# Optimization experiments

Measured on AMD Instinct MI355X. Metric: run time of the kernel, lower is better.

## Reference

```python
import jax, jax.numpy as jnp
import numpy as np

PATCH_NUMS = (10, 20, 30, 40)   # action_dim=10 * (1,2,3,4)
L = sum(PATCH_NUMS)             # 100
FIRST_L = PATCH_NUMS[0]         # 10
C = 768; NH = 12; HD = C // NH; DEPTH = 8; V = 4096; CVAE = 32; OBS = 23; TO = 1
EPS = 1e-6
STD = 0.02

LVL = np.concatenate([np.full(pn, i, dtype=np.int64) for i, pn in enumerate(PATCH_NUMS)])  # [L]
ATTN_BIAS = np.where(LVL[:, None] >= LVL[None, :], 0.0, -np.inf).astype(np.float32)       # [L, L] block-causal


def _ln(x):
    # LayerNorm without affine (eps=1e-6), as in norm_layer(..., elementwise_affine=False)
    m = x.mean(-1, keepdims=True)
    v = ((x - m) ** 2).mean(-1, keepdims=True)
    return (x - m) / jnp.sqrt(v + EPS)


def setup_inputs() -> dict:
    key = jax.random.key(0)
    ks = iter(jax.random.split(key, 40))
    B = 128
    p = {}
    p["nobs"] = jax.random.normal(next(ks), (B, TO, OBS), jnp.float32)
    p["x_BLCv_wo_first_l"] = jax.random.normal(next(ks), (B, L - FIRST_L, CVAE), jnp.float32)
    p["obs_w"] = jax.random.normal(next(ks), (OBS * TO, C), jnp.float32) * STD
    p["obs_b"] = jnp.zeros((C,), jnp.float32)
    p["word_w"] = jax.random.normal(next(ks), (CVAE, C), jnp.float32) * STD
    p["word_b"] = jnp.zeros((C,), jnp.float32)
    p["pos_start"] = jax.random.normal(next(ks), (1, FIRST_L, C), jnp.float32) * STD
    p["pos_1LC"] = jax.random.normal(next(ks), (1, L, C), jnp.float32) * STD
    p["lvl_emb"] = jax.random.normal(next(ks), (len(PATCH_NUMS), C), jnp.float32) * STD
    p["ada_w"] = jax.random.normal(next(ks), (DEPTH, C, 6 * C), jnp.float32) * STD
    p["ada_b"] = jnp.zeros((DEPTH, 6 * C), jnp.float32)
    p["qkv_w"] = jax.random.normal(next(ks), (DEPTH, C, 3 * C), jnp.float32) * STD
    p["qkv_b"] = jnp.zeros((DEPTH, 3 * C), jnp.float32)
    p["proj_w"] = jax.random.normal(next(ks), (DEPTH, C, C), jnp.float32) * STD
    p["proj_b"] = jnp.zeros((DEPTH, C), jnp.float32)
    p["fc1_w"] = jax.random.normal(next(ks), (DEPTH, C, 4 * C), jnp.float32) * STD
    p["fc1_b"] = jnp.zeros((DEPTH, 4 * C), jnp.float32)
    p["fc2_w"] = jax.random.normal(next(ks), (DEPTH, 4 * C, C), jnp.float32) * STD
    p["fc2_b"] = jnp.zeros((DEPTH, C), jnp.float32)
    p["hnm_w"] = jax.random.normal(next(ks), (C, 2 * C), jnp.float32) * STD
    p["hnm_b"] = jnp.zeros((2 * C,), jnp.float32)
    p["head_w"] = jax.random.normal(next(ks), (C, V), jnp.float32) * STD
    p["head_b"] = jnp.zeros((V,), jnp.float32)
    return p


def reference(nobs, x_BLCv_wo_first_l, obs_w, obs_b, word_w, word_b, pos_start, pos_1LC,
              lvl_emb, ada_w, ada_b, qkv_w, qkv_b, proj_w, proj_b, fc1_w, fc1_b,
              fc2_w, fc2_b, hnm_w, hnm_b, head_w, head_b):
    B = x_BLCv_wo_first_l.shape[0]
    feat = nobs[:, :TO].reshape(B, -1)                     # [B, obs_dim*To]
    cond = feat @ obs_w + obs_b                            # [B, C] (= sos = cond_BD)
    sos = cond[:, None, :] + pos_start                     # [B, first_l, C]
    x = jnp.concatenate([sos, x_BLCv_wo_first_l @ word_w + word_b], axis=1)  # [B, L, C]
    x = x + lvl_emb[jnp.asarray(LVL)][None] + pos_1LC      # lvl + positional embed
    bias = jnp.asarray(ATTN_BIAS)                          # [L, L]
    cond_s = jax.nn.silu(cond)                             # shared SiLU input to each block's ada_lin
    scale = HD ** -0.5
    for i in range(DEPTH):
        ada = (cond_s @ ada_w[i] + ada_b[i]).reshape(B, 1, 6, C)
        g1, g2, s1, s2, sh1, sh2 = (ada[:, :, j] for j in range(6))
        h = _ln(x) * (s1 + 1.0) + sh1
        qkv = (h @ qkv_w[i] + qkv_b[i]).reshape(B, L, 3, NH, HD)
        q, k, v = qkv[:, :, 0], qkv[:, :, 1], qkv[:, :, 2]
        att = jnp.einsum('bqhd,bkhd->bhqk', q, k) * scale
        att = jax.nn.softmax(att + bias, axis=-1)
        o = jnp.einsum('bhqk,bkhd->bqhd', att, v).reshape(B, L, C)
        x = x + (o @ proj_w[i] + proj_b[i]) * g1
        h = _ln(x) * (s2 + 1.0) + sh2
        h = jax.nn.gelu(h @ fc1_w[i] + fc1_b[i]) @ fc2_w[i] + fc2_b[i]
        x = x + h * g2
    # AdaLNBeforeHead + head
    hd = (cond_s @ hnm_w + hnm_b).reshape(B, 1, 2, C)
    x = _ln(x) * (hd[:, :, 0] + 1.0) + hd[:, :, 1]
    return x @ head_w + head_b                             # [B, L, V]
```

## Files before the change

### kernel.cpp

```cpp
#include <hip/hip_runtime.h>
#include <hip/hip_bf16.h>

typedef unsigned short u16;
typedef unsigned int u32;
typedef __attribute__((ext_vector_type(8))) short bf16x8;
typedef __attribute__((ext_vector_type(4))) float f32x4;

#define GLDS(gptr, lptr) __builtin_amdgcn_global_load_lds( \
    (const __attribute__((address_space(1))) u32*)(gptr), \
    (__attribute__((address_space(3))) u32*)(lptr), 16, 0, 0)

__device__ __forceinline__ float bf2f(u16 x) {
  union { float f; u32 u; } c; c.u = ((u32)x) << 16; return c.f;
}
__device__ __forceinline__ u16 f2bf(float f) {
  union { float f; u32 u; } c; c.f = f;
  u32 u = c.u;
  return (u16)((u + 0x7FFFu + ((u >> 16) & 1u)) >> 16);
}
__device__ __forceinline__ uint2 pack_bf4(f32x4 v) {
  uint2 pk;
  pk.x = ((u32)f2bf(v[1]) << 16) | (u32)f2bf(v[0]);
  pk.y = ((u32)f2bf(v[3]) << 16) | (u32)f2bf(v[2]);
  return pk;
}
__device__ __forceinline__ float gelu1(float v) {
  float t = 0.7978845608028654f * (v + 0.044715f * v * v * v);
  t = fminf(fmaxf(t, -15.f), 15.f);
  float e = __expf(2.f * t);
  return 0.5f * v * (1.f + (e - 1.f) / (e + 1.f));
}

template<int EPI>
__global__ __launch_bounds__(256)
void gemm64_kernel(const u16* __restrict__ A, const u16* __restrict__ Bt,
                   const float* __restrict__ bias,
                   u16* __restrict__ outb, float* __restrict__ outf,
                   float* __restrict__ xres, const float* __restrict__ gate, int gstride,
                   int M, int N, int K)
{
  __shared__ u16 ldsA[2][128 * 64];
  __shared__ u16 ldsB[2][128 * 64];
  const int tid = threadIdx.x;
  const int nX = N >> 7;

  int nwg = gridDim.x;
  int orig = blockIdx.x;
  int q = nwg >> 3, r = nwg & 7;
  int xcd = orig & 7, jj = orig >> 3;
  int wg = (xcd < r ? xcd * (q + 1) : r * (q + 1) + (xcd - r) * q) + jj;
  const int m0 = (wg / nX) << 7;
  const int n0 = (wg % nX) << 7;

  const int wid = tid >> 6, lane = tid & 63;
  const int wm = wid >> 1, wn = wid & 1;
  const int lr = lane & 15, lg = lane >> 4;

  f32x4 acc[4][4];
  #pragma unroll
  for (int i = 0; i < 4; ++i)
    #pragma unroll
    for (int j = 0; j < 4; ++j)
      acc[i][j] = (f32x4){0.f, 0.f, 0.f, 0.f};

  const int KT = K >> 6;
  int cur = 0;

  #define STAGE64(buf, kt) do { \
    int k0_ = (kt) << 6; \
    _Pragma("unroll") \
    for (int iss = 0; iss < 4; ++iss) { \
      int f_ = iss * 256 + tid; \
      int row_ = f_ >> 3, gl_ = f_ & 7; \
      int g_ = gl_ ^ (row_ & 7); \
      GLDS(A + (size_t)(m0 + row_) * K + k0_ + g_ * 8, &ldsA[buf][f_ * 8]); \
      GLDS(Bt + (size_t)(n0 + row_) * K + k0_ + g_ * 8, &ldsB[buf][f_ * 8]); \
    } \
  } while (0)

  STAGE64(0, 0);
  __syncthreads();
  for (int kt = 0; kt < KT; ++kt) {
    if (kt + 1 < KT) STAGE64(cur ^ 1, kt + 1);
    #pragma unroll
    for (int kk = 0; kk < 2; ++kk) {
      bf16x8 af[4], bv[4];
      #pragma unroll
      for (int i = 0; i < 4; ++i) {
        int ra = wm * 64 + i * 16 + lr;
        int da = kk * 4 + lg;
        af[i] = *(const bf16x8*)&ldsA[cur][(ra * 8 + (da ^ (ra & 7))) * 8];
        int rb = wn * 64 + i * 16 + lr;
        bv[i] = *(const bf16x8*)&ldsB[cur][(rb * 8 + (da ^ (rb & 7))) * 8];
      }
      #pragma unroll
      for (int mi = 0; mi < 4; ++mi)
        #pragma unroll
        for (int ni = 0; ni < 4; ++ni)
          acc[mi][ni] = __builtin_amdgcn_mfma_f32_16x16x32_bf16(bv[ni], af[mi], acc[mi][ni], 0, 0, 0);
    }
    __syncthreads();
    cur ^= 1;
  }
  #undef STAGE64

  f32x4 b4[4];
  #pragma unroll
  for (int ni = 0; ni < 4; ++ni)
    b4[ni] = *(const f32x4*)&bias[n0 + wn * 64 + ni * 16 + lg * 4];

  #pragma unroll
  for (int mi = 0; mi < 4; ++mi) {
    int row = m0 + wm * 64 + mi * 16 + lr;
    int bb = row / 100;
    #pragma unroll
    for (int ni = 0; ni < 4; ++ni) {
      int col = n0 + wn * 64 + ni * 16 + lg * 4;
      f32x4 v = acc[mi][ni] + b4[ni];
      size_t idx = (size_t)row * N + col;
      if (EPI == 0) {
        *(f32x4*)&outf[idx] = v;
      } else if (EPI == 1) {
        *(uint2*)&outb[idx] = pack_bf4(v);
      } else if (EPI == 2) {
        f32x4 g;
        #pragma unroll
        for (int e = 0; e < 4; ++e) g[e] = gelu1(v[e]);
        *(uint2*)&outb[idx] = pack_bf4(g);
      } else {
        f32x4 g4 = *(const f32x4*)&gate[(size_t)bb * gstride + col];
        f32x4 xr = *(f32x4*)&xres[idx];
        xr += v * g4;
        *(f32x4*)&xres[idx] = xr;
      }
    }
  }
}

template<int EPI>
__global__ __launch_bounds__(256)
void gemm_kernel(const u16* __restrict__ A, const u16* __restrict__ Bt,
                 const float* __restrict__ bias,
                 u16* __restrict__ outb, float* __restrict__ outf,
                 float* __restrict__ xres, const float* __restrict__ gate, int gstride,
                 int M, int N, int K)
{
  __shared__ u16 ldsA[2][128 * 32];
  __shared__ u16 ldsB[2][128 * 32];
  const int tid = threadIdx.x;
  const int nX = N >> 7;

  int nwg = gridDim.x;
  int orig = blockIdx.x;
  int q = nwg >> 3, r = nwg & 7;
  int xcd = orig & 7, jj = orig >> 3;
  int wg = (xcd < r ? xcd * (q + 1) : r * (q + 1) + (xcd - r) * q) + jj;
  const int m0 = (wg / nX) << 7;
  const int n0 = (wg % nX) << 7;

  const int wid = tid >> 6, lane = tid & 63;
  const int wm = wid >> 1, wn = wid & 1;
  const int lr = lane & 15, lg = lane >> 4;

  f32x4 acc[4][4];
  #pragma unroll
  for (int i = 0; i < 4; ++i)
    #pragma unroll
    for (int j = 0; j < 4; ++j)
      acc[i][j] = (f32x4){0.f, 0.f, 0.f, 0.f};

  const int KT = K >> 5;
  int cur = 0;

  #define STAGE(buf, kt) do { \
    int k0_ = (kt) << 5; \
    _Pragma("unroll") \
    for (int iss = 0; iss < 2; ++iss) { \
      int f_ = iss * 256 + tid; \
      int row_ = f_ >> 2, gl_ = f_ & 3; \
      int g_ = gl_ ^ (row_ & 3); \
      GLDS(A + (size_t)(m0 + row_) * K + k0_ + g_ * 8, &ldsA[buf][f_ * 8]); \
      GLDS(Bt + (size_t)(n0 + row_) * K + k0_ + g_ * 8, &ldsB[buf][f_ * 8]); \
    } \
  } while (0)

  STAGE(0, 0);
  __syncthreads();
  for (int kt = 0; kt < KT; ++kt) {
    if (kt + 1 < KT) STAGE(cur ^ 1, kt + 1);
    bf16x8 af[4], bfr[4];
    #pragma unroll
    for (int i = 0; i < 4; ++i) {
      int ra = wm * 64 + i * 16 + lr;
      af[i] = *(const bf16x8*)&ldsA[cur][(ra * 4 + (lg ^ (ra & 3))) * 8];
      int rb = wn * 64 + i * 16 + lr;
      bfr[i] = *(const bf16x8*)&ldsB[cur][(rb * 4 + (lg ^ (rb & 3))) * 8];
    }
    #pragma unroll
    for (int mi = 0; mi < 4; ++mi)
      #pragma unroll
      for (int ni = 0; ni < 4; ++ni)
        acc[mi][ni] = __builtin_amdgcn_mfma_f32_16x16x32_bf16(bfr[ni], af[mi], acc[mi][ni], 0, 0, 0);
    __syncthreads();
    cur ^= 1;
  }
  #undef STAGE

  f32x4 b4[4];
  #pragma unroll
  for (int ni = 0; ni < 4; ++ni)
    b4[ni] = *(const f32x4*)&bias[n0 + wn * 64 + ni * 16 + lg * 4];

  #pragma unroll
  for (int mi = 0; mi < 4; ++mi) {
    int row = m0 + wm * 64 + mi * 16 + lr;
    int bb = row / 100;
    #pragma unroll
    for (int ni = 0; ni < 4; ++ni) {
      int col = n0 + wn * 64 + ni * 16 + lg * 4;
      f32x4 v = acc[mi][ni] + b4[ni];
      size_t idx = (size_t)row * N + col;
      if (EPI == 0) {
        *(f32x4*)&outf[idx] = v;
      } else if (EPI == 1) {
        *(uint2*)&outb[idx] = pack_bf4(v);
      } else if (EPI == 2) {
        f32x4 g;
        #pragma unroll
        for (int e = 0; e < 4; ++e) g[e] = gelu1(v[e]);
        *(uint2*)&outb[idx] = pack_bf4(g);
      } else {
        f32x4 g4 = *(const f32x4*)&gate[(size_t)bb * gstride + col];
        f32x4 xr = *(f32x4*)&xres[idx];
        xr += v * g4;
        *(f32x4*)&xres[idx] = xr;
      }
    }
  }
}

__global__ __launch_bounds__(256)
void attn_kernel(const u16* __restrict__ qkv, u16* __restrict__ o)
{
  __shared__ u16 Qs[896 * 8];
  __shared__ u16 Ks[896 * 8];
  __shared__ u16 Vt[1024 * 8];
  __shared__ u16 Pl[4][256 * 8];
  const int tid = threadIdx.x;
  const int b = blockIdx.x / 12;
  const int h = blockIdx.x % 12;
  const int wid = tid >> 6, lane = tid & 63;
  const int lr = lane & 15, lg = lane >> 4;
  const size_t qbase = (size_t)b * 100 * 2304 + h * 64;

  #pragma unroll
  for (int i = 0; i < 16; ++i)
    ((u32*)Pl)[i * 256 + tid] = 0u;

  for (int it = 0; it < 3; ++it) {
    int idx = it * 256 + tid;
    int row = idx >> 3, gl = idx & 7;
    int g = gl ^ (row & 7);
    int sr = row < 100 ? row : 99;
    const u16* gq = qkv + qbase + (size_t)sr * 2304 + g * 8;
    GLDS(gq, &Qs[idx * 8]);
    GLDS(gq + 768, &Ks[idx * 8]);
  }
  if (tid < 128) {
    int idx = 768 + tid;
    int row = idx >> 3, gl = idx & 7;
    int g = gl ^ (row & 7);
    int sr = row < 100 ? row : 99;
    const u16* gq = qkv + qbase + (size_t)sr * 2304 + g * 8;
    GLDS(gq, &Qs[idx * 8]);
    GLDS(gq + 768, &Ks[idx * 8]);
  }

  for (int it = 0; it < 4; ++it) {
    int idx = it * 256 + tid;
    if (idx < 896) {
      int k = idx >> 3, gd = idx & 7;
      int sk = k < 100 ? k : 99;
      const u16* gv = qkv + qbase + (size_t)sk * 2304 + 1536 + gd * 8;
      u16 vv[8];
      *(uint4*)vv = *(const uint4*)gv;
      #pragma unroll
      for (int e = 0; e < 8; ++e) {
        int d = gd * 8 + e;
        Vt[(d * 16 + ((k >> 3) ^ (d & 15))) * 8 + (k & 7)] = vv[e];
      }
    }
  }
  __syncthreads();

  for (int s = wid; s < 7; s += 4) {
    f32x4 sa[7];
    #pragma unroll
    for (int nt = 0; nt < 7; ++nt) sa[nt] = (f32x4){0.f, 0.f, 0.f, 0.f};
    #pragma unroll
    for (int kk = 0; kk < 2; ++kk) {
      int qrow = s * 16 + lr;
      int qg = kk * 4 + lg;
      bf16x8 qa = *(const bf16x8*)&Qs[(qrow * 8 + (qg ^ (qrow & 7))) * 8];
      #pragma unroll
      for (int nt = 0; nt < 7; ++nt) {
        int krow = nt * 16 + lr;
        bf16x8 kb = *(const bf16x8*)&Ks[(krow * 8 + (qg ^ (krow & 7))) * 8];
        sa[nt] = __builtin_amdgcn_mfma_f32_16x16x32_bf16(qa, kb, sa[nt], 0, 0, 0);
      }
    }
    float pr[7][4];
    #pragma unroll
    for (int r = 0; r < 4; ++r) {
      int qq = s * 16 + lg * 4 + r;
      int kmax = qq < 10 ? 10 : qq < 30 ? 30 : qq < 60 ? 60 : 100;
      float m = -1e30f;
      #pragma unroll
      for (int nt = 0; nt < 7; ++nt) {
        int col = nt * 16 + lr;
        float sv = (col < kmax) ? sa[nt][r] * 0.125f : -1e30f;
        pr[nt][r] = sv;
        m = fmaxf(m, sv);
      }
      m = fmaxf(m, __shfl_xor(m, 1));
      m = fmaxf(m, __shfl_xor(m, 2));
      m = fmaxf(m, __shfl_xor(m, 4));
      m = fmaxf(m, __shfl_xor(m, 8));
      float sum = 0.f;
      #pragma unroll
      for (int nt = 0; nt < 7; ++nt) {
        float e = (pr[nt][r] > -1e29f) ? __expf(pr[nt][r] - m) : 0.f;
        pr[nt][r] = e;
        sum += e;
      }
      sum += __shfl_xor(sum, 1);
      sum += __shfl_xor(sum, 2);
      sum += __shfl_xor(sum, 4);
      sum += __shfl_xor(sum, 8);
      float inv = 1.f / sum;
      #pragma unroll
      for (int nt = 0; nt < 7; ++nt) pr[nt][r] *= inv;
    }
    #pragma unroll
    for (int nt = 0; nt < 7; ++nt) {
      int cg = nt * 2 + (lr >> 3);
      int e = lane & 7;
      #pragma unroll
      for (int r = 0; r < 4; ++r) {
        int row = lg * 4 + r;
        Pl[wid][(row * 16 + (cg ^ row)) * 8 + e] = f2bf(pr[nt][r]);
      }
    }
    asm volatile("s_waitcnt lgkmcnt(0)" ::: "memory");
    f32x4 oa[4];
    #pragma unroll
    for (int i = 0; i < 4; ++i) oa[i] = (f32x4){0.f, 0.f, 0.f, 0.f};
    #pragma unroll
    for (int kk = 0; kk < 4; ++kk) {
      int prow = lr;
      int pg = kk * 4 + lg;
      bf16x8 pa = *(const bf16x8*)&Pl[wid][(prow * 16 + (pg ^ prow)) * 8];
      #pragma unroll
      for (int nt = 0; nt < 4; ++nt) {
        int vrow = nt * 16 + lr;
        bf16x8 vb = *(const bf16x8*)&Vt[(vrow * 16 + (pg ^ (vrow & 15))) * 8];
        oa[nt] = __builtin_amdgcn_mfma_f32_16x16x32_bf16(vb, pa, oa[nt], 0, 0, 0);
      }
    }
    int qq = s * 16 + lr;
    if (qq < 100) {
      #pragma unroll
      for (int nt = 0; nt < 4; ++nt) {
        int d = nt * 16 + lg * 4;
        *(uint2*)&o[(size_t)(b * 100 + qq) * 768 + h * 64 + d] = pack_bf4(oa[nt]);
      }
    }
  }
}

__global__ __launch_bounds__(256)
void transpose_cast(const float* __restrict__ in, u16* __restrict__ out, int K, int N)
{
  __shared__ float tile[32][33];
  size_t zo = (size_t)blockIdx.z * K * N;
  const float* ip = in + zo;
  u16* op = out + zo;
  int n0 = blockIdx.x * 32, k0 = blockIdx.y * 32;
  int tx = threadIdx.x & 31, ty = threadIdx.x >> 5;
  #pragma unroll
  for (int i = 0; i < 32; i += 8)
    tile[ty + i][tx] = ip[(size_t)(k0 + ty + i) * N + n0 + tx];
  __syncthreads();
  #pragma unroll
  for (int i = 0; i < 32; i += 8)
    op[(size_t)(n0 + ty + i) * K + k0 + tx] = f2bf(tile[tx][ty + i]);
}

__global__ __launch_bounds__(256)
void cond_kernel(const float* __restrict__ nobs, const float* __restrict__ obs_w,
                 const float* __restrict__ obs_b, float* __restrict__ cond,
                 u16* __restrict__ cond_s)
{
  int idx = blockIdx.x * 256 + threadIdx.x;
  int b = idx / 768, c = idx - b * 768;
  float acc = obs_b[c];
  #pragma unroll
  for (int i = 0; i < 23; ++i)
    acc += nobs[b * 23 + i] * obs_w[i * 768 + c];
  cond[idx] = acc;
  float sg = acc / (1.f + __expf(-acc));
  cond_s[idx] = f2bf(sg);
}

__global__ __launch_bounds__(256)
void cast_bf16_kernel(const float* __restrict__ in, u16* __restrict__ out, int n)
{
  int idx = blockIdx.x * 256 + threadIdx.x;
  if (idx < n) out[idx] = f2bf(in[idx]);
}

__global__ __launch_bounds__(256)
void build_x_kernel(const float* __restrict__ cond, const float* __restrict__ pos_start,
                    const float* __restrict__ xw, const float* __restrict__ lvl_emb,
                    const float* __restrict__ pos_1LC, float* __restrict__ x)
{
  int idx = blockIdx.x * 256 + threadIdx.x;
  int row = idx / 768, c = idx - row * 768;
  int b = row / 100, l = row - b * 100;
  int lvl = l < 10 ? 0 : l < 30 ? 1 : l < 60 ? 2 : 3;
  float v;
  if (l < 10) v = cond[b * 768 + c] + pos_start[l * 768 + c];
  else        v = xw[(size_t)(b * 90 + (l - 10)) * 768 + c];
  x[idx] = v + lvl_emb[lvl * 768 + c] + pos_1LC[l * 768 + c];
}

__global__ __launch_bounds__(256)
void ln_mod_kernel(const float* __restrict__ x, const float* __restrict__ scale_b,
                   const float* __restrict__ shift_b, int stride, u16* __restrict__ h)
{
  int row = blockIdx.x;
  const float* xr = x + (size_t)row * 768;
  int t = threadIdx.x;
  float v0 = xr[t], v1 = xr[t + 256], v2 = xr[t + 512];
  float s = v0 + v1 + v2;
  float qv = v0 * v0 + v1 * v1 + v2 * v2;
  #pragma unroll
  for (int o = 32; o > 0; o >>= 1) {
    s += __shfl_down(s, o);
    qv += __shfl_down(qv, o);
  }
  __shared__ float red[4][2];
  if ((t & 63) == 0) { red[t >> 6][0] = s; red[t >> 6][1] = qv; }
  __syncthreads();
  float S = red[0][0] + red[1][0] + red[2][0] + red[3][0];
  float Q = red[0][1] + red[1][1] + red[2][1] + red[3][1];
  float mean = S * (1.f / 768.f);
  float var = Q * (1.f / 768.f) - mean * mean;
  float rstd = rsqrtf(var + 1e-6f);
  int bb = row / 100;
  const float* sc = scale_b + (size_t)bb * stride;
  const float* sh = shift_b + (size_t)bb * stride;
  u16* hr = h + (size_t)row * 768;
  hr[t]       = f2bf((v0 - mean) * rstd * (1.f + sc[t])       + sh[t]);
  hr[t + 256] = f2bf((v1 - mean) * rstd * (1.f + sc[t + 256]) + sh[t + 256]);
  hr[t + 512] = f2bf((v2 - mean) * rstd * (1.f + sc[t + 512]) + sh[t + 512]);
}

extern "C" void kernel_launch(void* const* d_in, const int* in_sizes, int n_in,
                              void* d_out, int out_size, void* d_ws, size_t ws_size,
                              hipStream_t stream)
{
  (void)in_sizes; (void)n_in; (void)out_size;
  const float* nobs      = (const float*)d_in[0];
  const float* xv        = (const float*)d_in[1];
  const float* obs_w     = (const float*)d_in[2];
  const float* obs_b     = (const float*)d_in[3];
  const float* word_w    = (const float*)d_in[4];
  const float* word_b    = (const float*)d_in[5];
  const float* pos_start = (const float*)d_in[6];
  const float* pos_1LC   = (const float*)d_in[7];
  const float* lvl_emb   = (const float*)d_in[8];
  const float* ada_w     = (const float*)d_in[9];
  const float* ada_b     = (const float*)d_in[10];
  const float* qkv_w     = (const float*)d_in[11];
  const float* qkv_b     = (const float*)d_in[12];
  const float* proj_w    = (const float*)d_in[13];
  const float* proj_b    = (const float*)d_in[14];
  const float* fc1_w     = (const float*)d_in[15];
  const float* fc1_b     = (const float*)d_in[16];
  const float* fc2_w     = (const float*)d_in[17];
  const float* fc2_b     = (const float*)d_in[18];
  const float* hnm_w     = (const float*)d_in[19];
  const float* hnm_b     = (const float*)d_in[20];
  const float* head_w    = (const float*)d_in[21];
  const float* head_b    = (const float*)d_in[22];
  float* out = (float*)d_out;

  const size_t NEED_BIG = 358000000;
  const bool bigAda = ws_size >= NEED_BIG;
  const int adaStride = bigAda ? 36864 : 4608;

  char* p = (char*)d_ws;
  auto take = [&](size_t bytes) { char* r = p; p += (bytes + 255) & ~(size_t)255; return r; };
  u16* Wword   = (u16*)take((size_t)768 * 32 * 2);
  u16* Wada    = (u16*)take((size_t)8 * 4608 * 768 * 2);
  u16* Wqkv    = (u16*)take((size_t)8 * 2304 * 768 * 2);
  u16* Wproj   = (u16*)take((size_t)8 * 768 * 768 * 2);
  u16* Wfc1    = (u16*)take((size_t)8 * 3072 * 768 * 2);
  u16* Wfc2    = (u16*)take((size_t)8 * 768 * 3072 * 2);
  u16* Whnm    = (u16*)take((size_t)1536 * 768 * 2);
  u16* Whead   = (u16*)take((size_t)4096 * 768 * 2);
  float* condf = (float*)take((size_t)128 * 768 * 4);
  u16* conds   = (u16*)take((size_t)128 * 768 * 2);
  u16* xvb     = (u16*)take((size_t)368640 * 2);
  float* xbuf  = (float*)take((size_t)12800 * 768 * 4);
  u16* hbuf    = (u16*)take((size_t)12800 * 768 * 2);
  float* adab  = (float*)take((size_t)128 * (size_t)adaStride * 4);
  u16* obuf    = (u16*)take((size_t)12800 * 768 * 2);
  float* hdbuf = (float*)take((size_t)128 * 1536 * 4);
  char* big    = take((size_t)12800 * 3072 * 2);
  float* xw  = (float*)big;
  u16* qkvb  = (u16*)big;
  u16* fc1b  = (u16*)big;

  transpose_cast<<<dim3(24, 1, 1),   256, 0, stream>>>(word_w, Wword, 32, 768);
  transpose_cast<<<dim3(144, 24, 8), 256, 0, stream>>>(ada_w,  Wada,  768, 4608);
  transpose_cast<<<dim3(72, 24, 8),  256, 0, stream>>>(qkv_w,  Wqkv,  768, 2304);
  transpose_cast<<<dim3(24, 24, 8),  256, 0, stream>>>(proj_w, Wproj, 768, 768);
  transpose_cast<<<dim3(96, 24, 8),  256, 0, stream>>>(fc1_w,  Wfc1,  768, 3072);
  transpose_cast<<<dim3(24, 96, 8),  256, 0, stream>>>(fc2_w,  Wfc2,  3072, 768);
  transpose_cast<<<dim3(48, 24, 1),  256, 0, stream>>>(hnm_w,  Whnm,  768, 1536);
  transpose_cast<<<dim3(128, 24, 1), 256, 0, stream>>>(head_w, Whead, 768, 4096);

  cond_kernel<<<384, 256, 0, stream>>>(nobs, obs_w, obs_b, condf, conds);
  cast_bf16_kernel<<<1440, 256, 0, stream>>>(xv, xvb, 368640);
  gemm_kernel<0><<<dim3(90 * 6), 256, 0, stream>>>(xvb, Wword, word_b,
      nullptr, xw, nullptr, nullptr, 0, 11520, 768, 32);
  build_x_kernel<<<38400, 256, 0, stream>>>(condf, pos_start, xw, lvl_emb, pos_1LC, xbuf);

  if (bigAda)
    gemm64_kernel<0><<<dim3(288), 256, 0, stream>>>(conds, Wada, ada_b,
        nullptr, adab, nullptr, nullptr, 0, 128, 36864, 768);

  for (int i = 0; i < 8; ++i) {
    if (!bigAda)
      gemm64_kernel<0><<<dim3(36), 256, 0, stream>>>(conds, Wada + (size_t)i * 4608 * 768,
          ada_b + (size_t)i * 4608, nullptr, adab, nullptr, nullptr, 0, 128, 4608, 768);
    float* adaL = bigAda ? adab + (size_t)i * 4608 : adab;
    ln_mod_kernel<<<12800, 256, 0, stream>>>(xbuf, adaL + 2 * 768, adaL + 4 * 768, adaStride, hbuf);
    gemm64_kernel<1><<<dim3(100 * 18), 256, 0, stream>>>(hbuf, Wqkv + (size_t)i * 2304 * 768,
        qkv_b + (size_t)i * 2304, qkvb, nullptr, nullptr, nullptr, 0, 12800, 2304, 768);
    attn_kernel<<<1536, 256, 0, stream>>>(qkvb, obuf);
    gemm64_kernel<3><<<dim3(100 * 6), 256, 0, stream>>>(obuf, Wproj + (size_t)i * 768 * 768,
        proj_b + (size_t)i * 768, nullptr, nullptr, xbuf, adaL + 0 * 768, adaStride, 12800, 768, 768);
    ln_mod_kernel<<<12800, 256, 0, stream>>>(xbuf, adaL + 3 * 768, adaL + 5 * 768, adaStride, hbuf);
    gemm64_kernel<2><<<dim3(100 * 24), 256, 0, stream>>>(hbuf, Wfc1 + (size_t)i * 3072 * 768,
        fc1_b + (size_t)i * 3072, fc1b, nullptr, nullptr, nullptr, 0, 12800, 3072, 768);
    gemm64_kernel<3><<<dim3(100 * 6), 256, 0, stream>>>(fc1b, Wfc2 + (size_t)i * 768 * 3072,
        fc2_b + (size_t)i * 768, nullptr, nullptr, xbuf, adaL + 1 * 768, adaStride, 12800, 768, 3072);
  }

  gemm_kernel<0><<<dim3(12), 256, 0, stream>>>(conds, Whnm, hnm_b,
      nullptr, hdbuf, nullptr, nullptr, 0, 128, 1536, 768);
  ln_mod_kernel<<<12800, 256, 0, stream>>>(xbuf, hdbuf, hdbuf + 768, 1536, hbuf);
  gemm64_kernel<0><<<dim3(100 * 32), 256, 0, stream>>>(hbuf, Whead, head_b,
      nullptr, out, nullptr, nullptr, 0, 12800, 4096, 768);
}
```

Before: 3.260 ms.

## Drop XCD-aware tile remap in GEMMs and vectorize LayerNorm to one wave per row

The GEMM kernels stop remapping block IDs across XCDs and take the tile coordinates directly from a 2D grid. LayerNorm-modulate now handles one row per wavefront, four rows per block, using float4 loads, a pure shuffle reduction with no LDS or barrier, and packed bf16 stores. The LayerNorm part targets launch overhead and narrow scalar memory traffic. Removing the XCD swizzle may change L2 locality, since neighbouring tiles that share A or B panels can end up on different XCD caches.

Measured after the change: 3.223 ms. About the same (-1.1%).

```diff
diff --git a/kernel.cpp b/kernel.cpp
--- a/kernel.cpp
+++ b/kernel.cpp
@@ -42,15 +42,8 @@
   __shared__ u16 ldsA[2][128 * 64];
   __shared__ u16 ldsB[2][128 * 64];
   const int tid = threadIdx.x;
-  const int nX = N >> 7;
-
-  int nwg = gridDim.x;
-  int orig = blockIdx.x;
-  int q = nwg >> 3, r = nwg & 7;
-  int xcd = orig & 7, jj = orig >> 3;
-  int wg = (xcd < r ? xcd * (q + 1) : r * (q + 1) + (xcd - r) * q) + jj;
-  const int m0 = (wg / nX) << 7;
-  const int n0 = (wg % nX) << 7;
+  const int m0 = blockIdx.y << 7;
+  const int n0 = blockIdx.x << 7;
 
   const int wid = tid >> 6, lane = tid & 63;
   const int wm = wid >> 1, wn = wid & 1;
@@ -148,15 +141,8 @@
   __shared__ u16 ldsA[2][128 * 32];
   __shared__ u16 ldsB[2][128 * 32];
   const int tid = threadIdx.x;
-  const int nX = N >> 7;
-
-  int nwg = gridDim.x;
-  int orig = blockIdx.x;
-  int q = nwg >> 3, r = nwg & 7;
-  int xcd = orig & 7, jj = orig >> 3;
-  int wg = (xcd < r ? xcd * (q + 1) : r * (q + 1) + (xcd - r) * q) + jj;
-  const int m0 = (wg / nX) << 7;
-  const int n0 = (wg % nX) << 7;
+  const int m0 = blockIdx.y << 7;
+  const int n0 = blockIdx.x << 7;
 
   const int wid = tid >> 6, lane = tid & 63;
   const int wm = wid >> 1, wn = wid & 1;
@@ -438,32 +424,44 @@
 void ln_mod_kernel(const float* __restrict__ x, const float* __restrict__ scale_b,
                    const float* __restrict__ shift_b, int stride, u16* __restrict__ h)
 {
-  int row = blockIdx.x;
+  const int tid = threadIdx.x;
+  const int wid = tid >> 6, lane = tid & 63;
+  const int row = blockIdx.x * 4 + wid;
   const float* xr = x + (size_t)row * 768;
-  int t = threadIdx.x;
-  float v0 = xr[t], v1 = xr[t + 256], v2 = xr[t + 512];
-  float s = v0 + v1 + v2;
-  float qv = v0 * v0 + v1 * v1 + v2 * v2;
+
+  f32x4 v[3];
+  #pragma unroll
+  for (int c = 0; c < 3; ++c)
+    v[c] = *(const f32x4*)&xr[c * 256 + lane * 4];
+
+  float s = 0.f, qv = 0.f;
+  #pragma unroll
+  for (int c = 0; c < 3; ++c)
+    #pragma unroll
+    for (int e = 0; e < 4; ++e) { s += v[c][e]; qv += v[c][e] * v[c][e]; }
   #pragma unroll
   for (int o = 32; o > 0; o >>= 1) {
-    s += __shfl_down(s, o);
-    qv += __shfl_down(qv, o);
-  }
-  __shared__ float red[4][2];
-  if ((t & 63) == 0) { red[t >> 6][0] = s; red[t >> 6][1] = qv; }
-  __syncthreads();
-  float S = red[0][0] + red[1][0] + red[2][0] + red[3][0];
-  float Q = red[0][1] + red[1][1] + red[2][1] + red[3][1];
-  float mean = S * (1.f / 768.f);
-  float var = Q * (1.f / 768.f) - mean * mean;
+    s += __shfl_xor(s, o);
+    qv += __shfl_xor(qv, o);
+  }
+  float mean = s * (1.f / 768.f);
+  float var = qv * (1.f / 768.f) - mean * mean;
   float rstd = rsqrtf(var + 1e-6f);
-  int bb = row / 100;
+
+  const int bb = row / 100;
   const float* sc = scale_b + (size_t)bb * stride;
   const float* sh = shift_b + (size_t)bb * stride;
   u16* hr = h + (size_t)row * 768;
-  hr[t]       = f2bf((v0 - mean) * rstd * (1.f + sc[t])       + sh[t]);
-  hr[t + 256] = f2bf((v1 - mean) * rstd * (1.f + sc[t + 256]) + sh[t + 256]);
-  hr[t + 512] = f2bf((v2 - mean) * rstd * (1.f + sc[t + 512]) + sh[t + 512]);
+  #pragma unroll
+  for (int c = 0; c < 3; ++c) {
+    f32x4 s4 = *(const f32x4*)&sc[c * 256 + lane * 4];
+    f32x4 h4 = *(const f32x4*)&sh[c * 256 + lane * 4];
+    f32x4 o4;
+    #pragma unroll
+    for (int e = 0; e < 4; ++e)
+      o4[e] = (v[c][e] - mean) * rstd * (1.f + s4[e]) + h4[e];
+    *(uint2*)&hr[c * 256 + lane * 4] = pack_bf4(o4);
+  }
 }
 
 extern "C" void kernel_launch(void* const* d_in, const int* in_sizes, int n_in,
@@ -534,35 +532,35 @@
 
   cond_kernel<<<384, 256, 0, stream>>>(nobs, obs_w, obs_b, condf, conds);
   cast_bf16_kernel<<<1440, 256, 0, stream>>>(xv, xvb, 368640);
-  gemm_kernel<0><<<dim3(90 * 6), 256, 0, stream>>>(xvb, Wword, word_b,
+  gemm_kernel<0><<<dim3(6, 90), 256, 0, stream>>>(xvb, Wword, word_b,
       nullptr, xw, nullptr, nullptr, 0, 11520, 768, 32);
   build_x_kernel<<<38400, 256, 0, stream>>>(condf, pos_start, xw, lvl_emb, pos_1LC, xbuf);
 
   if (bigAda)
-    gemm64_kernel<0><<<dim3(288), 256, 0, stream>>>(conds, Wada, ada_b,
+    gemm64_kernel<0><<<dim3(288, 1), 256, 0, stream>>>(conds, Wada, ada_b,
         nullptr, adab, nullptr, nullptr, 0, 128, 36864, 768);
 
   for (int i = 0; i < 8; ++i) {
     if (!bigAda)
-      gemm64_kernel<0><<<dim3(36), 256, 0, stream>>>(conds, Wada + (size_t)i * 4608 * 768,
+      gemm64_kernel<0><<<dim3(36, 1), 256, 0, stream>>>(conds, Wada + (size_t)i * 4608 * 768,
           ada_b + (size_t)i * 4608, nullptr, adab, nullptr, nullptr, 0, 128, 4608, 768);
     float* adaL = bigAda ? adab + (size_t)i * 4608 : adab;
-    ln_mod_kernel<<<12800, 256, 0, stream>>>(xbuf, adaL + 2 * 768, adaL + 4 * 768, adaStride, hbuf);
-    gemm64_kernel<1><<<dim3(100 * 18), 256, 0, stream>>>(hbuf, Wqkv + (size_t)i * 2304 * 768,
+    ln_mod_kernel<<<3200, 256, 0, stream>>>(xbuf, adaL + 2 * 768, adaL + 4 * 768, adaStride, hbuf);
+    gemm64_kernel<1><<<dim3(18, 100), 256, 0, stream>>>(hbuf, Wqkv + (size_t)i * 2304 * 768,
         qkv_b + (size_t)i * 2304, qkvb, nullptr, nullptr, nullptr, 0, 12800, 2304, 768);
     attn_kernel<<<1536, 256, 0, stream>>>(qkvb, obuf);
-    gemm64_kernel<3><<<dim3(100 * 6), 256, 0, stream>>>(obuf, Wproj + (size_t)i * 768 * 768,
+    gemm64_kernel<3><<<dim3(6, 100), 256, 0, stream>>>(obuf, Wproj + (size_t)i * 768 * 768,
         proj_b + (size_t)i * 768, nullptr, nullptr, xbuf, adaL + 0 * 768, adaStride, 12800, 768, 768);
-    ln_mod_kernel<<<12800, 256, 0, stream>>>(xbuf, adaL + 3 * 768, adaL + 5 * 768, adaStride, hbuf);
-    gemm64_kernel<2><<<dim3(100 * 24), 256, 0, stream>>>(hbuf, Wfc1 + (size_t)i * 3072 * 768,
+    ln_mod_kernel<<<3200, 256, 0, stream>>>(xbuf, adaL + 3 * 768, adaL + 5 * 768, adaStride, hbuf);
+    gemm64_kernel<2><<<dim3(24, 100), 256, 0, stream>>>(hbuf, Wfc1 + (size_t)i * 3072 * 768,
         fc1_b + (size_t)i * 3072, fc1b, nullptr, nullptr, nullptr, 0, 12800, 3072, 768);
-    gemm64_kernel<3><<<dim3(100 * 6), 256, 0, stream>>>(fc1b, Wfc2 + (size_t)i * 768 * 3072,
+    gemm64_kernel<3><<<dim3(6, 100), 256, 0, stream>>>(fc1b, Wfc2 + (size_t)i * 768 * 3072,
         fc2_b + (size_t)i * 768, nullptr, nullptr, xbuf, adaL + 1 * 768, adaStride, 12800, 768, 3072);
   }
 
-  gemm_kernel<0><<<dim3(12), 256, 0, stream>>>(conds, Whnm, hnm_b,
+  gemm_kernel<0><<<dim3(12, 1), 256, 0, stream>>>(conds, Whnm, hnm_b,
       nullptr, hdbuf, nullptr, nullptr, 0, 128, 1536, 768);
-  ln_mod_kernel<<<12800, 256, 0, stream>>>(xbuf, hdbuf, hdbuf + 768, 1536, hbuf);
-  gemm64_kernel<0><<<dim3(100 * 32), 256, 0, stream>>>(hbuf, Whead, head_b,
+  ln_mod_kernel<<<3200, 256, 0, stream>>>(xbuf, hdbuf, hdbuf + 768, 1536, hbuf);
+  gemm64_kernel<0><<<dim3(32, 100), 256, 0, stream>>>(hbuf, Whead, head_b,
       nullptr, out, nullptr, nullptr, 0, 12800, 4096, 768);
 }
```
